# Optimization experiments

Hardware: AMD Instinct MI355X
Metric: run time of the kernel (lower is better)

Reference implementation:

```python
import jax, jax.numpy as jnp
import numpy as np

N_STREAMS = 4
DIM = 256
TMAX = 20
RMS_EPS = 1e-05
SK_EPS = 1e-08


def sinkhorn_knopp(logits):
    # logits: [B, T, n, n]; tmax fixed iterations of row/col normalization
    x = logits.astype(jnp.float32)
    x = x - jnp.max(x, axis=(-2, -1), keepdims=True)
    x = jnp.exp(x)
    for _ in range(TMAX):
        x = x / (jnp.sum(x, axis=-2, keepdims=True) + SK_EPS)
        x = x / (jnp.sum(x, axis=-1, keepdims=True) + SK_EPS)
    return x.astype(logits.dtype)


def setup_inputs() -> dict:
    key = jax.random.key(0)
    ks = jax.random.split(key, 5)
    B, T, n, C = 8, 4096, N_STREAMS, DIM
    nc = n * C
    x_streams = jax.random.normal(ks[0], (B, T, n, C), dtype=jnp.float32)
    scale = jnp.ones((nc,), dtype=jnp.float32)
    lim = 1.0 / np.sqrt(nc)
    w_pre = jax.random.uniform(ks[1], (n, nc), minval=-lim, maxval=lim, dtype=jnp.float32)
    w_post = jax.random.uniform(ks[2], (n, nc), minval=-lim, maxval=lim, dtype=jnp.float32)
    w_res = jax.random.uniform(ks[3], (n * n, nc), minval=-lim, maxval=lim, dtype=jnp.float32)
    return {
        "x_streams": x_streams,
        "scale": scale,
        "w_pre": w_pre,
        "w_post": w_post,
        "w_res": w_res,
        "alpha_pre": jnp.float32(0.01),
        "alpha_post": jnp.float32(0.01),
        "alpha_res": jnp.float32(0.01),
        "b_pre": jnp.zeros((n,), dtype=jnp.float32),
        "b_post": jnp.zeros((n,), dtype=jnp.float32),
        "b_res": jnp.zeros((n * n,), dtype=jnp.float32),
    }


def reference(x_streams, scale, w_pre, w_post, w_res,
              alpha_pre, alpha_post, alpha_res, b_pre, b_post, b_res):
    B, T, n, C = x_streams.shape
    x_flat = x_streams.reshape(B, T, n * C)
    # RMSNorm over flattened stream dim
    rms = jnp.mean(x_flat * x_flat, axis=-1, keepdims=True)
    x_norm = x_flat * jax.lax.rsqrt(rms + RMS_EPS) * scale
    # routing projections (Linear with no bias == x @ W.T)
    h_pre = jax.nn.sigmoid(alpha_pre * (x_norm @ w_pre.T) + b_pre)          # [B,T,n]
    h_post = 2.0 * jax.nn.sigmoid(alpha_post * (x_norm @ w_post.T) + b_post)  # [B,T,n]
    h_res = (alpha_res * (x_norm @ w_res.T) + b_res).reshape(B, T, n, n)
    h_res = sinkhorn_knopp(h_res)
    # mixing
    x_in = jnp.einsum('btn,btnc->btc', h_pre, x_streams)   # pre-mix (residual = Identity)
    y = x_in
    resmix = jnp.einsum('btij,btjc->btic', h_res, x_streams)
    addy = h_post[..., None] * y[..., None, :]
    return resmix + addy
```

## Files before the change

### kernel.cpp

```cpp
#include <hip/hip_runtime.h>
#include <math.h>

#define G 8

__device__ __forceinline__ float sigmoidf_(float s) {
    return 1.0f / (1.0f + __expf(-s));
}

__device__ __forceinline__ float fold_(float X, float Y, int m, int l) {
    const bool hi = (l & m) != 0;
    const float a = hi ? Y : X;
    const float b = hi ? X : Y;
    return a + __shfl_xor(b, m);
}

__global__ __launch_bounds__(512)
__attribute__((amdgpu_waves_per_eu(4, 8)))
void fused_route_mix(const float* __restrict__ x,
                     const float* __restrict__ scale,
                     const float* __restrict__ w_pre,
                     const float* __restrict__ w_post,
                     const float* __restrict__ w_res,
                     const float* __restrict__ ap_p,
                     const float* __restrict__ apo_p,
                     const float* __restrict__ ar_p,
                     const float* __restrict__ b_pre,
                     const float* __restrict__ b_post,
                     const float* __restrict__ b_res,
                     float* __restrict__ out,
                     int rounds)
{
    __shared__ __align__(16) float xs[G * 1024];
    __shared__ __align__(16) float hraw[G * 24];
    __shared__ float sslds[G];
    __shared__ __align__(16) float Mlds[G * 16];

    const int t = threadIdx.x;
    const int w = t >> 6;
    const int l = t & 63;

    float wreg[3][16];
    #pragma unroll
    for (int rr = 0; rr < 3; ++rr) {
        const int k = 3 * w + rr;
        const float* wp = (k < 4) ? (w_pre + (size_t)k * 1024)
                        : (k < 8) ? (w_post + (size_t)(k - 4) * 1024)
                                  : (w_res + (size_t)(k - 8) * 1024);
        #pragma unroll
        for (int mp = 0; mp < 4; ++mp)
            #pragma unroll
            for (int j = 0; j < 4; ++j)
                wreg[rr][4 * mp + j] =
                    wp[4 * l + 256 * mp + j] * scale[4 * l + 256 * mp + j];
    }

    const float a_pre = ap_p[0], a_post = apo_p[0], a_res = ar_p[0];
    float4* const xs4 = (float4*)xs;

    for (int r = blockIdx.x; r < rounds; r += gridDim.x) {
        const size_t base = (size_t)r * (G * 1024);
        const float4* __restrict__ xg = (const float4*)(x + base);

        asm volatile("s_waitcnt lgkmcnt(0)\n\ts_barrier" ::: "memory");

        #pragma unroll 2
        for (int i = 0; i < G; ++i) {
            float p0 = 0.f, p1 = 0.f, p2 = 0.f, ss = 0.f;
            const bool stage = (i == w);
            #pragma unroll
            for (int mp = 0; mp < 4; ++mp) {
                const float4 xv = xg[(i << 8) + (mp << 6) + l];
                if (stage)
                    xs4[(i << 8) + (mp << 6) + l] = xv;
                const float xe[4] = {xv.x, xv.y, xv.z, xv.w};
                #pragma unroll
                for (int j = 0; j < 4; ++j) {
                    const float xj = xe[j];
                    p0 = fmaf(xj, wreg[0][4 * mp + j], p0);
                    p1 = fmaf(xj, wreg[1][4 * mp + j], p1);
                    p2 = fmaf(xj, wreg[2][4 * mp + j], p2);
                    ss = fmaf(xj, xj, ss);
                }
            }
            const float q0 = fold_(p0, p1, 32, l);
            const float q1 = fold_(p2, ss, 32, l);
            float s = fold_(q0, q1, 16, l);
            s += __shfl_xor(s, 8);
            s += __shfl_xor(s, 4);
            s += __shfl_xor(s, 2);
            s += __shfl_xor(s, 1);
            if ((l & 15) == 0) {
                const int vid = ((l >> 5) & 1) | (((l >> 4) & 1) << 1);
                if (vid < 3) hraw[i * 24 + 3 * w + vid] = s;
                else if (w == 0) sslds[i] = s;
            }
        }

        asm volatile("s_waitcnt lgkmcnt(0)\n\ts_barrier" ::: "memory");

        if (w == 0) {
            const int tk = l & (G - 1);
            const float inv = rsqrtf(sslds[tk] * (1.0f / 1024.0f) + 1e-5f);
            float hr[24];
            const float4* __restrict__ hp = (const float4*)(hraw + tk * 24);
            #pragma unroll
            for (int q = 0; q < 6; ++q) {
                const float4 hv = hp[q];
                hr[4 * q + 0] = hv.x; hr[4 * q + 1] = hv.y;
                hr[4 * q + 2] = hv.z; hr[4 * q + 3] = hv.w;
            }

            float hpre[4], hpost[4];
            #pragma unroll
            for (int j = 0; j < 4; ++j)
                hpre[j] = sigmoidf_(fmaf(a_pre * inv, hr[j], b_pre[j]));
            #pragma unroll
            for (int i = 0; i < 4; ++i)
                hpost[i] = 2.0f * sigmoidf_(fmaf(a_post * inv, hr[4 + i], b_post[i]));

            float K[4][4];
            float mx = -1e30f;
            #pragma unroll
            for (int i = 0; i < 4; ++i)
                #pragma unroll
                for (int j = 0; j < 4; ++j) {
                    const float vv = fmaf(a_res * inv, hr[8 + 4 * i + j], b_res[4 * i + j]);
                    K[i][j] = vv;
                    mx = fmaxf(mx, vv);
                }
            #pragma unroll
            for (int i = 0; i < 4; ++i)
                #pragma unroll
                for (int j = 0; j < 4; ++j)
                    K[i][j] = __expf(K[i][j] - mx);

            float u[4] = {1.f, 1.f, 1.f, 1.f};
            float v[4] = {1.f, 1.f, 1.f, 1.f};
            for (int it = 0; it < 20; ++it) {
                #pragma unroll
                for (int j = 0; j < 4; ++j) {
                    const float S = (fmaf(u[0], K[0][j], u[1] * K[1][j]))
                                  + (fmaf(u[2], K[2][j], u[3] * K[3][j]));
                    v[j] = v[j] * __builtin_amdgcn_rcpf(fmaf(v[j], S, 1e-8f));
                }
                #pragma unroll
                for (int i = 0; i < 4; ++i) {
                    const float T = (fmaf(K[i][0], v[0], K[i][1] * v[1]))
                                  + (fmaf(K[i][2], v[2], K[i][3] * v[3]));
                    u[i] = u[i] * __builtin_amdgcn_rcpf(fmaf(u[i], T, 1e-8f));
                }
            }

            if (l < G) {
                float4* Md = (float4*)(Mlds + (l << 4));
                #pragma unroll
                for (int i2 = 0; i2 < 4; ++i2) {
                    float4 row;
                    row.x = fmaf(u[i2] * K[i2][0], v[0], hpost[i2] * hpre[0]);
                    row.y = fmaf(u[i2] * K[i2][1], v[1], hpost[i2] * hpre[1]);
                    row.z = fmaf(u[i2] * K[i2][2], v[2], hpost[i2] * hpre[2]);
                    row.w = fmaf(u[i2] * K[i2][3], v[3], hpost[i2] * hpre[3]);
                    Md[i2] = row;
                }
            }
        }

        asm volatile("s_waitcnt lgkmcnt(0)\n\ts_barrier" ::: "memory");

        const int s4 = w & 3;
        const int ihalf = w >> 2;
        #pragma unroll 2
        for (int ii = 0; ii < 4; ++ii) {
            const int i = (ii << 1) + ihalf;
            const float4 m4 = ((const float4*)Mlds)[(i << 2) + s4];
            const float4* __restrict__ xt = xs4 + (i << 8);
            const float4 a0 = xt[0 * 64 + l];
            const float4 a1 = xt[1 * 64 + l];
            const float4 a2 = xt[2 * 64 + l];
            const float4 a3 = xt[3 * 64 + l];
            float4 o;
            o.x = m4.x * a0.x + m4.y * a1.x + m4.z * a2.x + m4.w * a3.x;
            o.y = m4.x * a0.y + m4.y * a1.y + m4.z * a2.y + m4.w * a3.y;
            o.z = m4.x * a0.z + m4.y * a1.z + m4.z * a2.z + m4.w * a3.z;
            o.w = m4.x * a0.w + m4.y * a1.w + m4.z * a2.w + m4.w * a3.w;
            ((float4*)(out + base))[(i << 8) + (s4 << 6) + l] = o;
        }
    }
}

extern "C" void kernel_launch(void* const* d_in, const int* in_sizes, int n_in,
                              void* d_out, int out_size, void* d_ws, size_t ws_size,
                              hipStream_t stream) {
    const float* x      = (const float*)d_in[0];
    const float* scale  = (const float*)d_in[1];
    const float* w_pre  = (const float*)d_in[2];
    const float* w_post = (const float*)d_in[3];
    const float* w_res  = (const float*)d_in[4];
    const float* a_pre  = (const float*)d_in[5];
    const float* a_post = (const float*)d_in[6];
    const float* a_res  = (const float*)d_in[7];
    const float* b_pre  = (const float*)d_in[8];
    const float* b_post = (const float*)d_in[9];
    const float* b_res  = (const float*)d_in[10];
    float* out = (float*)d_out;

    const int tokens = in_sizes[0] / 1024;
    const int rounds = tokens / G;
    const int grid = rounds < 1024 ? rounds : 1024;

    fused_route_mix<<<grid, 512, 0, stream>>>(
        x, scale, w_pre, w_post, w_res,
        a_pre, a_post, a_res, b_pre, b_post, b_res,
        out, rounds);
}
```

Before: 308.5 us.

## Split fused routing/mixing kernel into separate route and mix kernels

Unfuses the single kernel into a routing kernel, which computes the per-token 4x4 mixing matrices into workspace memory, and a separate mix kernel that rereads x to apply them. The routing kernel no longer stages x in LDS, double-buffers its small reduction scratch, rotates which wave runs Sinkhorn, and processes 16 tokens per round, which removes one barrier per round. The aim is to drop the large LDS footprint and the serial Sinkhorn stall between stages so occupancy and overlap improve. The cost is reading x from global memory twice (about 128MB extra traffic) plus a second launch and writes of the matrix buffer.

```diff
diff --git a/kernel.cpp b/kernel.cpp
--- a/kernel.cpp
+++ b/kernel.cpp
@@ -1,7 +1,8 @@
 #include <hip/hip_runtime.h>
 #include <math.h>
 
-#define G 8
+
+#define GA 16
 
 __device__ __forceinline__ float sigmoidf_(float s) {
     return 1.0f / (1.0f + __expf(-s));
@@ -16,24 +17,21 @@
 
 __global__ __launch_bounds__(512)
 __attribute__((amdgpu_waves_per_eu(4, 8)))
-void fused_route_mix(const float* __restrict__ x,
-                     const float* __restrict__ scale,
-                     const float* __restrict__ w_pre,
-                     const float* __restrict__ w_post,
-                     const float* __restrict__ w_res,
-                     const float* __restrict__ ap_p,
-                     const float* __restrict__ apo_p,
-                     const float* __restrict__ ar_p,
-                     const float* __restrict__ b_pre,
-                     const float* __restrict__ b_post,
-                     const float* __restrict__ b_res,
-                     float* __restrict__ out,
-                     int rounds)
+void route_k(const float* __restrict__ x,
+             const float* __restrict__ scale,
+             const float* __restrict__ w_pre,
+             const float* __restrict__ w_post,
+             const float* __restrict__ w_res,
+             const float* __restrict__ ap_p,
+             const float* __restrict__ apo_p,
+             const float* __restrict__ ar_p,
+             const float* __restrict__ b_pre,
+             const float* __restrict__ b_post,
+             const float* __restrict__ b_res,
+             float* __restrict__ Mout,
+             int rounds)
 {
-    __shared__ __align__(16) float xs[G * 1024];
-    __shared__ __align__(16) float hraw[G * 24];
-    __shared__ float sslds[G];
-    __shared__ __align__(16) float Mlds[G * 16];
+    __shared__ float hraw[2][GA * 28];
 
     const int t = threadIdx.x;
     const int w = t >> 6;
@@ -54,24 +52,17 @@
                     wp[4 * l + 256 * mp + j] * scale[4 * l + 256 * mp + j];
     }
 
-    const float a_pre = ap_p[0], a_post = apo_p[0], a_res = ar_p[0];
-    float4* const xs4 = (float4*)xs;
-
-    for (int r = blockIdx.x; r < rounds; r += gridDim.x) {
-        const size_t base = (size_t)r * (G * 1024);
-        const float4* __restrict__ xg = (const float4*)(x + base);
-
-        asm volatile("s_waitcnt lgkmcnt(0)\n\ts_barrier" ::: "memory");
+    int lr = 0;
+    for (int r = blockIdx.x; r < rounds; r += gridDim.x, ++lr) {
+        const float4* __restrict__ xg = (const float4*)(x + (size_t)r * (GA * 1024));
+        float* __restrict__ hb = hraw[lr & 1];
 
         #pragma unroll 2
-        for (int i = 0; i < G; ++i) {
+        for (int i = 0; i < GA; ++i) {
             float p0 = 0.f, p1 = 0.f, p2 = 0.f, ss = 0.f;
-            const bool stage = (i == w);
             #pragma unroll
             for (int mp = 0; mp < 4; ++mp) {
                 const float4 xv = xg[(i << 8) + (mp << 6) + l];
-                if (stage)
-                    xs4[(i << 8) + (mp << 6) + l] = xv;
                 const float xe[4] = {xv.x, xv.y, xv.z, xv.w};
                 #pragma unroll
                 for (int j = 0; j < 4; ++j) {
@@ -91,24 +82,25 @@
             s += __shfl_xor(s, 1);
             if ((l & 15) == 0) {
                 const int vid = ((l >> 5) & 1) | (((l >> 4) & 1) << 1);
-                if (vid < 3) hraw[i * 24 + 3 * w + vid] = s;
-                else if (w == 0) sslds[i] = s;
+                if (vid < 3) hb[i * 28 + 3 * w + vid] = s;
+                else if (w == 0) hb[i * 28 + 24] = s;
             }
         }
 
         asm volatile("s_waitcnt lgkmcnt(0)\n\ts_barrier" ::: "memory");
 
-        if (w == 0) {
-            const int tk = l & (G - 1);
-            const float inv = rsqrtf(sslds[tk] * (1.0f / 1024.0f) + 1e-5f);
+        if (w == (lr & 7)) {
+            const int tk = l & (GA - 1);
+            const float* __restrict__ hp = hb + tk * 28;
             float hr[24];
-            const float4* __restrict__ hp = (const float4*)(hraw + tk * 24);
             #pragma unroll
             for (int q = 0; q < 6; ++q) {
-                const float4 hv = hp[q];
+                const float4 hv = ((const float4*)hp)[q];
                 hr[4 * q + 0] = hv.x; hr[4 * q + 1] = hv.y;
                 hr[4 * q + 2] = hv.z; hr[4 * q + 3] = hv.w;
             }
+            const float inv = rsqrtf(hp[24] * (1.0f / 1024.0f) + 1e-5f);
+            const float a_pre = ap_p[0], a_post = apo_p[0], a_res = ar_p[0];
 
             float hpre[4], hpost[4];
             #pragma unroll
@@ -151,8 +143,9 @@
                 }
             }
 
-            if (l < G) {
-                float4* Md = (float4*)(Mlds + (l << 4));
+            if (l < GA) {
+                float4* __restrict__ Md =
+                    (float4*)(Mout + ((size_t)r * GA + tk) * 16);
                 #pragma unroll
                 for (int i2 = 0; i2 < 4; ++i2) {
                     float4 row;
@@ -164,27 +157,49 @@
                 }
             }
         }
-
-        asm volatile("s_waitcnt lgkmcnt(0)\n\ts_barrier" ::: "memory");
-
-        const int s4 = w & 3;
-        const int ihalf = w >> 2;
-        #pragma unroll 2
-        for (int ii = 0; ii < 4; ++ii) {
-            const int i = (ii << 1) + ihalf;
-            const float4 m4 = ((const float4*)Mlds)[(i << 2) + s4];
-            const float4* __restrict__ xt = xs4 + (i << 8);
-            const float4 a0 = xt[0 * 64 + l];
-            const float4 a1 = xt[1 * 64 + l];
-            const float4 a2 = xt[2 * 64 + l];
-            const float4 a3 = xt[3 * 64 + l];
-            float4 o;
-            o.x = m4.x * a0.x + m4.y * a1.x + m4.z * a2.x + m4.w * a3.x;
-            o.y = m4.x * a0.y + m4.y * a1.y + m4.z * a2.y + m4.w * a3.y;
-            o.z = m4.x * a0.z + m4.y * a1.z + m4.z * a2.z + m4.w * a3.z;
-            o.w = m4.x * a0.w + m4.y * a1.w + m4.z * a2.w + m4.w * a3.w;
-            ((float4*)(out + base))[(i << 8) + (s4 << 6) + l] = o;
-        }
+    }
+}
+
+__global__ __launch_bounds__(512)
+void mix_k(const float* __restrict__ x,
+           const float* __restrict__ M,
+           float* __restrict__ out,
+           int ntok)
+{
+    const int l = threadIdx.x & 63;
+    const int gw = (int)((blockIdx.x * 512u + threadIdx.x) >> 6);
+    const int nw = (int)((gridDim.x * 512u) >> 6);
+
+    for (int tok = gw; tok < ntok; tok += nw) {
+        const float4* __restrict__ xt = (const float4*)(x + (size_t)tok * 1024);
+        const float4* __restrict__ Mt = (const float4*)(M + (size_t)tok * 16);
+        const float4 m0 = Mt[0], m1 = Mt[1], m2 = Mt[2], m3 = Mt[3];
+        const float4 a0 = xt[0 * 64 + l];
+        const float4 a1 = xt[1 * 64 + l];
+        const float4 a2 = xt[2 * 64 + l];
+        const float4 a3 = xt[3 * 64 + l];
+        float4* __restrict__ ot = (float4*)(out + (size_t)tok * 1024);
+        float4 o0, o1, o2, o3;
+        o0.x = m0.x*a0.x + m0.y*a1.x + m0.z*a2.x + m0.w*a3.x;
+        o0.y = m0.x*a0.y + m0.y*a1.y + m0.z*a2.y + m0.w*a3.y;
+        o0.z = m0.x*a0.z + m0.y*a1.z + m0.z*a2.z + m0.w*a3.z;
+        o0.w = m0.x*a0.w + m0.y*a1.w + m0.z*a2.w + m0.w*a3.w;
+        o1.x = m1.x*a0.x + m1.y*a1.x + m1.z*a2.x + m1.w*a3.x;
+        o1.y = m1.x*a0.y + m1.y*a1.y + m1.z*a2.y + m1.w*a3.y;
+        o1.z = m1.x*a0.z + m1.y*a1.z + m1.z*a2.z + m1.w*a3.z;
+        o1.w = m1.x*a0.w + m1.y*a1.w + m1.z*a2.w + m1.w*a3.w;
+        o2.x = m2.x*a0.x + m2.y*a1.x + m2.z*a2.x + m2.w*a3.x;
+        o2.y = m2.x*a0.y + m2.y*a1.y + m2.z*a2.y + m2.w*a3.y;
+        o2.z = m2.x*a0.z + m2.y*a1.z + m2.z*a2.z + m2.w*a3.z;
+        o2.w = m2.x*a0.w + m2.y*a1.w + m2.z*a2.w + m2.w*a3.w;
+        o3.x = m3.x*a0.x + m3.y*a1.x + m3.z*a2.x + m3.w*a3.x;
+        o3.y = m3.x*a0.y + m3.y*a1.y + m3.z*a2.y + m3.w*a3.y;
+        o3.z = m3.x*a0.z + m3.y*a1.z + m3.z*a2.z + m3.w*a3.z;
+        o3.w = m3.x*a0.w + m3.y*a1.w + m3.z*a2.w + m3.w*a3.w;
+        ot[0 * 64 + l] = o0;
+        ot[1 * 64 + l] = o1;
+        ot[2 * 64 + l] = o2;
+        ot[3 * 64 + l] = o3;
     }
 }
 
@@ -202,14 +217,17 @@
     const float* b_pre  = (const float*)d_in[8];
     const float* b_post = (const float*)d_in[9];
     const float* b_res  = (const float*)d_in[10];
-    float* out = (float*)d_out;
+    float* out  = (float*)d_out;
+    float* Mbuf = (float*)d_ws;
 
     const int tokens = in_sizes[0] / 1024;
-    const int rounds = tokens / G;
-    const int grid = rounds < 1024 ? rounds : 1024;
-
-    fused_route_mix<<<grid, 512, 0, stream>>>(
+    const int roundsA = tokens / GA;
+    const int gridA = roundsA < 1024 ? roundsA : 1024;
+
+    route_k<<<gridA, 512, 0, stream>>>(
         x, scale, w_pre, w_post, w_res,
         a_pre, a_post, a_res, b_pre, b_post, b_res,
-        out, rounds);
-}
+        Mbuf, roundsA);
+
+    mix_k<<<1024, 512, 0, stream>>>(x, Mbuf, out, tokens);
+}
```

Result: no change. 304.6 us (-1.3%).
